# Optimization experiments

Hardware: AMD Instinct MI355X
Metric: run time of the kernel (lower is better)

## Reference

```python
import jax, jax.numpy as jnp
import numpy as np

N = 40000      # num_ent
INIT = 100     # init_dim
D = 200        # gcn_dim
F = 4          # num_factors
E = 800000     # num edges (incl. inverses)
NREL = 800     # num_rel * 2
L = 2          # gcn_layer
B = 2048       # batch of (sub, rel)
H2 = D // 2    # CLUBSample hidden_size // 2
NPAIR = F * (F - 1) // 2  # 6 MI discriminators


def setup_inputs() -> dict:
    key = jax.random.key(0)
    ks = jax.random.split(key, 24)
    inp = {}
    inp['sub'] = jax.random.randint(ks[0], (B,), 0, N)
    inp['rel'] = jax.random.randint(ks[1], (B,), 0, NREL)
    inp['edge_index'] = jax.random.randint(ks[2], (2, E), 0, N)
    inp['edge_type'] = jax.random.randint(ks[3], (E,), 0, NREL)
    inp['perm'] = jax.random.permutation(ks[4], B)
    s = 0.05
    inp['init_embed'] = jax.random.normal(ks[5], (N, INIT), jnp.float32) * s
    inp['init_rel'] = jax.random.normal(ks[6], (NREL, D), jnp.float32) * s
    stdv = 1.0 / np.sqrt(F * D)
    inp['pca_w'] = jax.random.uniform(ks[7], (INIT, F * D), jnp.float32, -stdv, stdv)
    inp['pca_b'] = jax.random.uniform(ks[8], (F * D,), jnp.float32, -stdv, stdv)
    inp['cw_w'] = jax.random.normal(ks[9], (D, D), jnp.float32) * 0.1
    inp['w_rel'] = jax.random.normal(ks[10], (L, D, D), jnp.float32) * s
    # CLUBSample MLPs stacked over the NPAIR discriminators
    inp['mu_w1'] = jax.random.normal(ks[11], (NPAIR, D, H2), jnp.float32) * s
    inp['mu_b1'] = jnp.zeros((NPAIR, H2), jnp.float32)
    inp['mu_w2'] = jax.random.normal(ks[12], (NPAIR, H2, D), jnp.float32) * s
    inp['mu_b2'] = jnp.zeros((NPAIR, D), jnp.float32)
    inp['lv_w1'] = jax.random.normal(ks[13], (NPAIR, D, H2), jnp.float32) * s
    inp['lv_b1'] = jnp.zeros((NPAIR, H2), jnp.float32)
    inp['lv_w2'] = jax.random.normal(ks[14], (NPAIR, H2, D), jnp.float32) * s
    inp['lv_b2'] = jnp.zeros((NPAIR, D), jnp.float32)
    return inp


def _leaky(v):
    return jnp.where(v > 0, v, 0.2 * v)


def _club(xi, yj, yj_perm, w1, b1, w2, b2, v1, c1, v2, c2):
    # CLUBSample.forward: MI upper bound between factor i and factor j
    mu = jax.nn.relu(xi @ w1 + b1) @ w2 + b2
    logvar = jnp.tanh(jax.nn.relu(xi @ v1 + c1) @ v2 + c2)
    inv_var = jnp.exp(-logvar)
    pos = -(mu - yj) ** 2 * inv_var
    neg = -(mu - yj_perm) ** 2 * inv_var
    return (pos.sum(-1) - neg.sum(-1)).mean() / 2.0


def _encode(init_embed, init_rel, pca_w, pca_b, cw_w, w_rel, edge_index, edge_type):
    # SparseInputLinear + tanh -> [N, F, D]
    x = jnp.tanh(init_embed @ pca_w + pca_b).reshape(N, F, D)
    # CalculateWeight: leaky_relu matmul then softmax over the factor axis
    kw = _leaky(x.reshape(-1, D) @ cw_w).reshape(N, F, D)
    kw = jax.nn.softmax(kw, axis=1)
    r = init_rel
    src, dst = edge_index[0], edge_index[1]
    for l in range(L):
        r_edge = r[edge_type]  # [E, D]
        aggs = []
        for k in range(F):  # small fixed loop over factors to bound memory
            m = x[src, k] * r_edge                              # [E, D] messages
            logit = _leaky(jnp.sum(m * x[dst, k], axis=-1))     # [E] attention logits
            mx = jax.ops.segment_max(logit, dst, num_segments=N)
            a = jnp.exp(logit - mx[dst])
            den = jax.ops.segment_sum(a, dst, num_segments=N)
            a = a / (den[dst] + 1e-16)                          # per-dst softmax
            aggs.append(jax.ops.segment_sum(a[:, None] * m, dst, num_segments=N))
        agg = jnp.stack(aggs, axis=1)                           # [N, F, D]
        x = jnp.tanh(agg) * kw                                  # factor routing
        r = r @ w_rel[l]
    return x, r


def reference(sub, rel, edge_index, edge_type, perm,
              init_embed, init_rel, pca_w, pca_b, cw_w, w_rel,
              mu_w1, mu_b1, mu_w2, mu_b2, lv_w1, lv_b1, lv_w2, lv_b2):
    x, _ = _encode(init_embed, init_rel, pca_w, pca_b, cw_w, w_rel, edge_index, edge_type)
    sub_emb = x[sub].reshape(B, F * D)
    rel_emb = jnp.tile(init_rel[rel], (1, F))  # index_select + repeat(1, F)
    mi_loss = jnp.float32(0.0)
    cnt = 0
    for i in range(F):
        for j in range(i + 1, F):
            xi = sub_emb[:, i * D:(i + 1) * D]
            yj = sub_emb[:, j * D:(j + 1) * D]
            mi_loss = mi_loss + _club(xi, yj, yj[perm],
                                      mu_w1[cnt], mu_b1[cnt], mu_w2[cnt], mu_b2[cnt],
                                      lv_w1[cnt], lv_b1[cnt], lv_w2[cnt], lv_b2[cnt])
            cnt += 1
    return (sub_emb, rel_emb, x, mi_loss)
```

## Files before the change

### kernel.cpp

```cpp
#include <hip/hip_runtime.h>
#include <hip/hip_bf16.h>

#define N_NODES 40000
#define INIT_D  100
#define DD      200
#define FF      4
#define EE      800000
#define NRELS   800
#define BB      2048
#define H2D     100
#define FD      800
#define RPAD    224
#define XPAD    256

typedef __hip_bfloat16 bf16;
typedef unsigned char u8;
typedef unsigned int u32;
typedef float floatx2 __attribute__((ext_vector_type(2)));
typedef float floatx4 __attribute__((ext_vector_type(4)));
typedef u32 u32x2 __attribute__((ext_vector_type(2)));

#define XSCALE 256.f
#define XINV   (1.f / 256.f)

__device__ __forceinline__ float b2f(bf16 v) { return __bfloat162float(v); }

__device__ __forceinline__ void fp8x4_dec(u32 q, float* o) {
    floatx2 lo = __builtin_amdgcn_cvt_pk_f32_fp8((int)q, false);
    floatx2 hi = __builtin_amdgcn_cvt_pk_f32_fp8((int)q, true);
    o[0] = lo.x; o[1] = lo.y; o[2] = hi.x; o[3] = hi.y;
}

__device__ __forceinline__ u32 fp8x4_enc(float v0, float v1, float v2, float v3) {
    int o = 0;
    o = __builtin_amdgcn_cvt_pk_fp8_f32(v0, v1, o, false);
    o = __builtin_amdgcn_cvt_pk_fp8_f32(v2, v3, o, true);
    return (u32)o;
}

__device__ __forceinline__ float red16(float v) {
    int t;
    t = __builtin_amdgcn_update_dpp(0, __float_as_int(v), 0xB1, 0xF, 0xF, true);
    v += __int_as_float(t);
    t = __builtin_amdgcn_update_dpp(0, __float_as_int(v), 0x4E, 0xF, 0xF, true);
    v += __int_as_float(t);
    t = __builtin_amdgcn_update_dpp(0, __float_as_int(v), 0x124, 0xF, 0xF, true);
    v += __int_as_float(t);
    t = __builtin_amdgcn_update_dpp(0, __float_as_int(v), 0x128, 0xF, 0xF, true);
    v += __int_as_float(t);
    return v;
}

__global__ __launch_bounds__(256) void zero_kernel(int* count, double* loss, u8* pad0, u8* pad1) {
    int idx = blockIdx.x * 256 + threadIdx.x;
    if (idx < N_NODES) count[idx] = 0;
    if (idx == 0) *loss = 0.0;
    if (idx < 64 && pad0) ((u32*)pad0)[idx] = 0u;
    if (idx < 64 && pad1) ((u32*)pad1)[idx] = 0u;
}

__global__ __launch_bounds__(64) void pca_kernel(const float* __restrict__ emb,
                                                 const float* __restrict__ pw,
                                                 const float* __restrict__ pb,
                                                 u8* __restrict__ xq,
                                                 float* __restrict__ xf,
                                                 int mode) {
    __shared__ float es[INIT_D][18];
    int r0 = blockIdx.y * 16;
    int c  = blockIdx.x * 64 + threadIdx.x;
    for (int idx = threadIdx.x; idx < 16 * INIT_D; idx += 64) {
        int r = idx / INIT_D, k = idx % INIT_D;
        es[k][r] = emb[(size_t)(r0 + r) * INIT_D + k];
    }
    __syncthreads();
    if (c >= FD) return;
    floatx2 acc[8];
#pragma unroll
    for (int i = 0; i < 8; i++) acc[i] = (floatx2){0.f, 0.f};
    for (int k = 0; k < INIT_D; k++) {
        float w = pw[k * FD + c];
        floatx2 w2 = (floatx2){w, w};
#pragma unroll
        for (int i = 0; i < 8; i++) acc[i] += *(const floatx2*)&es[k][2 * i] * w2;
    }
    float bias = pb[c];
#pragma unroll
    for (int r = 0; r < 16; r++) {
        float a = (r & 1) ? acc[r >> 1].y : acc[r >> 1].x;
        float v = tanhf(a + bias);
        if (mode == 0) {
            int t8 = __builtin_amdgcn_cvt_pk_fp8_f32(v * XSCALE, 0.f, 0, false);
            xq[(size_t)(r0 + r) * FD + c] = (u8)(t8 & 0xFF);
        } else {
            xf[(size_t)(r0 + r) * FD + c] = v;
        }
    }
}

__global__ __launch_bounds__(256) void kw_fast(const u8* __restrict__ xr,
                                               const float* __restrict__ cw,
                                               u8* __restrict__ kwout) {
    __shared__ float as[4][16][100];
    int wv = threadIdx.x >> 6, lane = threadIdx.x & 63;
    int g = blockIdx.x * 4 + wv;
    size_t rowbase = (size_t)g * 16;
    floatx2 acc[16][2];
#pragma unroll
    for (int r = 0; r < 16; r++) {
        acc[r][0] = (floatx2){0.f, 0.f};
        acc[r][1] = (floatx2){0.f, 0.f};
    }
    int cc[4], cl[4];
#pragma unroll
    for (int i = 0; i < 4; i++) { cc[i] = i * 64 + lane; cl[i] = cc[i] < DD ? cc[i] : DD - 1; }
    for (int kc = 0; kc < 2; kc++) {
        for (int j = lane; j < 400; j += 64) {
            int rr = j / 25, k4 = (j % 25) * 4;
            u32 q = *(const u32*)(xr + (rowbase + rr) * DD + kc * 100 + k4);
            float dv[4];
            fp8x4_dec(q, dv);
            *(floatx4*)&as[wv][rr][k4] = (floatx4){dv[0], dv[1], dv[2], dv[3]};
        }
        for (int kk = 0; kk < 100; kk += 4) {
            floatx2 w01[4], w23[4];
#pragma unroll
            for (int j = 0; j < 4; j++) {
                const float* cwp = cw + (size_t)(kc * 100 + kk + j) * DD;
                w01[j] = (floatx2){cwp[cl[0]], cwp[cl[1]]};
                w23[j] = (floatx2){cwp[cl[2]], cwp[cl[3]]};
            }
#pragma unroll
            for (int r = 0; r < 16; r++) {
                floatx4 av = *(const floatx4*)&as[wv][r][kk];
                acc[r][0] += av.x * w01[0]; acc[r][1] += av.x * w23[0];
                acc[r][0] += av.y * w01[1]; acc[r][1] += av.y * w23[1];
                acc[r][0] += av.z * w01[2]; acc[r][1] += av.z * w23[2];
                acc[r][0] += av.w * w01[3]; acc[r][1] += av.w * w23[3];
            }
        }
    }
#define GA(r, i) ((i) == 0 ? acc[r][0].x : (i) == 1 ? acc[r][0].y : (i) == 2 ? acc[r][1].x : acc[r][1].y)
#pragma unroll
    for (int j = 0; j < 4; j++) {
        int n = g * 4 + j;
#pragma unroll
        for (int i = 0; i < 4; i++) {
            if (cc[i] >= DD) continue;
            float v0 = GA(j * 4 + 0, i) * XINV, v1 = GA(j * 4 + 1, i) * XINV;
            float v2 = GA(j * 4 + 2, i) * XINV, v3 = GA(j * 4 + 3, i) * XINV;
            v0 = v0 > 0.f ? v0 : 0.2f * v0;
            v1 = v1 > 0.f ? v1 : 0.2f * v1;
            v2 = v2 > 0.f ? v2 : 0.2f * v2;
            v3 = v3 > 0.f ? v3 : 0.2f * v3;
            float m = fmaxf(fmaxf(v0, v1), fmaxf(v2, v3));
            float e0 = __expf(v0 - m), e1 = __expf(v1 - m);
            float e2 = __expf(v2 - m), e3 = __expf(v3 - m);
            float inv = 1.f / (e0 + e1 + e2 + e3);
            size_t base = (size_t)n * FD + cc[i];
            kwout[base]          = (u8)(e0 * inv * 255.f + 0.5f);
            kwout[base + DD]     = (u8)(e1 * inv * 255.f + 0.5f);
            kwout[base + 2 * DD] = (u8)(e2 * inv * 255.f + 0.5f);
            kwout[base + 3 * DD] = (u8)(e3 * inv * 255.f + 0.5f);
        }
    }
#undef GA
}

__global__ __launch_bounds__(256) void kw_old(const float* __restrict__ x,
                                              const float* __restrict__ cw,
                                              u8* __restrict__ kw) {
    int wave = threadIdx.x >> 6, lane = threadIdx.x & 63;
    int n = blockIdx.x * 4 + wave;
    const float* xp = x + (size_t)n * FD;
    float acc[4][4];
#pragma unroll
    for (int f = 0; f < 4; f++)
#pragma unroll
        for (int i = 0; i < 4; i++) acc[f][i] = 0.f;
    for (int k = 0; k < DD; k++) {
        float xv0 = xp[k], xv1 = xp[DD + k];
        float xv2 = xp[2 * DD + k], xv3 = xp[3 * DD + k];
#pragma unroll
        for (int i = 0; i < 4; i++) {
            int d = i * 64 + lane;
            float w = (d < DD) ? cw[k * DD + d] : 0.f;
            acc[0][i] += xv0 * w; acc[1][i] += xv1 * w;
            acc[2][i] += xv2 * w; acc[3][i] += xv3 * w;
        }
    }
    u8* kwp = kw + (size_t)n * FD;
#pragma unroll
    for (int i = 0; i < 4; i++) {
        int d = i * 64 + lane;
        if (d >= DD) continue;
        float v0 = acc[0][i], v1 = acc[1][i], v2 = acc[2][i], v3 = acc[3][i];
        v0 = v0 > 0.f ? v0 : 0.2f * v0;
        v1 = v1 > 0.f ? v1 : 0.2f * v1;
        v2 = v2 > 0.f ? v2 : 0.2f * v2;
        v3 = v3 > 0.f ? v3 : 0.2f * v3;
        float m = fmaxf(fmaxf(v0, v1), fmaxf(v2, v3));
        float e0 = __expf(v0 - m), e1 = __expf(v1 - m), e2 = __expf(v2 - m), e3 = __expf(v3 - m);
        float inv = 1.f / (e0 + e1 + e2 + e3);
        kwp[d]          = (u8)(e0 * inv * 255.f + 0.5f);
        kwp[DD + d]     = (u8)(e1 * inv * 255.f + 0.5f);
        kwp[2 * DD + d] = (u8)(e2 * inv * 255.f + 0.5f);
        kwp[3 * DD + d] = (u8)(e3 * inv * 255.f + 0.5f);
    }
}

__global__ __launch_bounds__(256) void count_kernel(const int* __restrict__ dst, int* count) {
    int e = blockIdx.x * 256 + threadIdx.x;
    atomicAdd(&count[dst[e]], 1);
}

__global__ __launch_bounds__(1024) void scan_kernel(int* __restrict__ count, int* __restrict__ offs) {
    __shared__ int wsums[16];
    __shared__ int carry_s;
    int tid = threadIdx.x;
    int wv = tid >> 6, lane = tid & 63;
    if (tid == 0) { carry_s = 0; offs[0] = 0; }
    __syncthreads();
    for (int base = 0; base < 40960; base += 1024) {
        int i = base + tid;
        int v = (i < N_NODES) ? count[i] : 0;
        if (i < N_NODES) count[i] = 0;
        int x = v;
#pragma unroll
        for (int off = 1; off < 64; off <<= 1) {
            int y = __shfl_up(x, off, 64);
            if (lane >= off) x += y;
        }
        if (lane == 63) wsums[wv] = x;
        __syncthreads();
        if (wv == 0) {
            int s = (lane < 16) ? wsums[lane] : 0;
#pragma unroll
            for (int off = 1; off < 16; off <<= 1) {
                int y = __shfl_up(s, off, 64);
                if (lane >= off) s += y;
            }
            if (lane < 16) wsums[lane] = s;
        }
        __syncthreads();
        int add = carry_s + (wv > 0 ? wsums[wv - 1] : 0);
        int incl = x + add;
        if (i < N_NODES) offs[i + 1] = incl;
        __syncthreads();
        if (tid == 1023) carry_s = incl;
        __syncthreads();
    }
}

__global__ __launch_bounds__(256) void scatter_kernel(const int* __restrict__ src,
                                                      const int* __restrict__ dst,
                                                      const int* __restrict__ etyp,
                                                      const int* __restrict__ offs,
                                                      int* cursor,
                                                      u32* __restrict__ ep) {
    int e = blockIdx.x * 256 + threadIdx.x;
    int d = dst[e];
    int p = offs[d] + atomicAdd(&cursor[d], 1);
    ep[p] = ((u32)etyp[e] << 16) | (u32)src[e];
}

__global__ __launch_bounds__(256) void r0pad_kernel(const float* __restrict__ r0,
                                                    float* __restrict__ rp) {
    int idx = blockIdx.x * 256 + threadIdx.x;
    int n = idx / RPAD, d = idx % RPAD;
    rp[idx] = (d < DD) ? r0[n * DD + d] : 0.f;
}

__global__ __launch_bounds__(256) void rmul_kernel(const float* __restrict__ r0,
                                                   const float* __restrict__ w,
                                                   float* __restrict__ r1) {
    __shared__ float row[DD];
    int n = blockIdx.x;
    if (threadIdx.x < DD) row[threadIdx.x] = r0[n * DD + threadIdx.x];
    __syncthreads();
    int d = threadIdx.x;
    if (d < DD) {
        float acc = 0.f;
        for (int k = 0; k < DD; k++) acc += row[k] * w[k * DD + d];
        r1[n * RPAD + d] = acc;
    } else if (d < RPAD) {
        r1[n * RPAD + d] = 0.f;
    }
}

__global__ __launch_bounds__(256) void agg_fp8(const u8* __restrict__ xin,
                                               const u8* __restrict__ kwv,
                                               const float* __restrict__ r,
                                               const int* __restrict__ offs,
                                               const u32* __restrict__ ep,
                                               u8* __restrict__ xoq,
                                               float* __restrict__ xof,
                                               int mode) {
    int n    = blockIdx.x * 4 + (threadIdx.x >> 6);
    int lane = threadIdx.x & 63;
    int f    = lane >> 4;
    int k    = lane & 15;
    bool act = k < 13;
    int xoff = f * DD + k * 16;
    int roffc = k * 16; if (roffc > 200) roffc = 200;

    float xdf[16];
    {
        const u8* xdp = xin + (size_t)n * FD + xoff;
        u32x2 a = *(const u32x2*)xdp;
        u32x2 b = *(const u32x2*)(xdp + 8);
        fp8x4_dec(a.x, xdf); fp8x4_dec(a.y, xdf + 4);
        fp8x4_dec(b.x, xdf + 8); fp8x4_dec(b.y, xdf + 12);
    }
    floatx2 xd2[8];
#pragma unroll
    for (int j = 0; j < 8; j++) xd2[j] = (floatx2){xdf[2 * j], xdf[2 * j + 1]};

    floatx2 A[8];
#pragma unroll
    for (int j = 0; j < 8; j++) A[j] = (floatx2){0.f, 0.f};
    float Sm = 0.f;

    int e0 = offs[n], e1 = offs[n + 1];

#define ISSUE(QA, QB, R0, R1, R2, R3, JJ) do {                                  \
    u32 wrd_ = (u32)__builtin_amdgcn_readlane((int)epv, (JJ));                  \
    int s_ = (int)(wrd_ & 0xFFFFu), t_ = (int)(wrd_ >> 16);                     \
    const u8* xsp_ = xin + (size_t)s_ * FD;                                     \
    const float* rp_ = r + (size_t)t_ * RPAD + roffc;                           \
    QA = *(const u32x2*)(xsp_ + xoff);                                          \
    QB = *(const u32x2*)(xsp_ + xoff + 8);                                      \
    const floatx4* r4_ = (const floatx4*)rp_;                                   \
    R0 = r4_[0]; R1 = r4_[1]; R2 = r4_[2]; R3 = r4_[3];                         \
} while (0)

#define COMPUTE(QA, QB, R0, R1, R2, R3) do {                                    \
    float xsf_[16];                                                             \
    fp8x4_dec(QA.x, xsf_);     fp8x4_dec(QA.y, xsf_ + 4);                       \
    fp8x4_dec(QB.x, xsf_ + 8); fp8x4_dec(QB.y, xsf_ + 12);                      \
    floatx2 rr_[8];                                                             \
    rr_[0] = (floatx2){R0.x, R0.y}; rr_[1] = (floatx2){R0.z, R0.w};             \
    rr_[2] = (floatx2){R1.x, R1.y}; rr_[3] = (floatx2){R1.z, R1.w};             \
    rr_[4] = (floatx2){R2.x, R2.y}; rr_[5] = (floatx2){R2.z, R2.w};             \
    rr_[6] = (floatx2){R3.x, R3.y}; rr_[7] = (floatx2){R3.z, R3.w};             \
    floatx2 mm_[8];                                                             \
    floatx2 ps_ = (floatx2){0.f, 0.f};                                          \
    _Pragma("unroll")                                                           \
    for (int j_ = 0; j_ < 8; j_++) {                                            \
        floatx2 xs2_ = (floatx2){xsf_[2 * j_], xsf_[2 * j_ + 1]};               \
        mm_[j_] = xs2_ * rr_[j_];                                               \
        ps_ += mm_[j_] * xd2[j_];                                               \
    }                                                                           \
    float p_ = red16(ps_.x + ps_.y);                                            \
    float q_ = p_ * (XINV * XINV);                                              \
    float lg_ = fmaxf(q_, 0.2f * q_);                                           \
    float wg_ = __expf(lg_);                                                    \
    Sm += wg_;                                                                  \
    floatx2 w2_ = (floatx2){wg_, wg_};                                          \
    _Pragma("unroll")                                                           \
    for (int j_ = 0; j_ < 8; j_++) A[j_] += w2_ * mm_[j_];                      \
} while (0)

    for (int cb = e0; cb < e1; cb += 64) {
        int cnt = e1 - cb; if (cnt > 64) cnt = 64;
        u32 epv = ep[cb + (lane < cnt ? lane : cnt - 1)];
        u32x2 qaA, qbA, qaB, qbB;
        floatx4 rA0, rA1, rA2, rA3, rB0, rB1, rB2, rB3;
        ISSUE(qaA, qbA, rA0, rA1, rA2, rA3, 0);
        if (cnt > 1) ISSUE(qaB, qbB, rB0, rB1, rB2, rB3, 1);
        int m2 = cnt & ~1;
        for (int ii = 0; ii < m2; ii += 2) {
            COMPUTE(qaA, qbA, rA0, rA1, rA2, rA3);
            if (ii + 2 < cnt) ISSUE(qaA, qbA, rA0, rA1, rA2, rA3, ii + 2);
            COMPUTE(qaB, qbB, rB0, rB1, rB2, rB3);
            if (ii + 3 < cnt) ISSUE(qaB, qbB, rB0, rB1, rB2, rB3, ii + 3);
        }
        if (cnt & 1) COMPUTE(qaA, qbA, rA0, rA1, rA2, rA3);
    }
#undef ISSUE
#undef COMPUTE

    float inv = 1.f / (Sm + 1e-16f);
    u32 kws[4];
    {
        const u8* kwp = kwv + (size_t)n * FD + xoff;
        u32x2 ka = *(const u32x2*)kwp;
        u32x2 kb = *(const u32x2*)(kwp + 8);
        kws[0] = ka.x; kws[1] = ka.y; kws[2] = kb.x; kws[3] = kb.y;
    }
    float v[16];
#pragma unroll
    for (int j = 0; j < 16; j++) {
        float kv = (float)((kws[j >> 2] >> ((j & 3) * 8)) & 0xFF) * (1.f / 255.f);
        float Aj = (j & 1) ? A[j >> 1].y : A[j >> 1].x;
        v[j] = tanhf(Aj * inv * XINV) * kv;
    }
    if (mode == 0) {
        if (act) {
            u32 o0 = fp8x4_enc(v[0] * XSCALE, v[1] * XSCALE, v[2] * XSCALE, v[3] * XSCALE);
            u32 o1 = fp8x4_enc(v[4] * XSCALE, v[5] * XSCALE, v[6] * XSCALE, v[7] * XSCALE);
            u32 o2 = fp8x4_enc(v[8] * XSCALE, v[9] * XSCALE, v[10] * XSCALE, v[11] * XSCALE);
            u32 o3 = fp8x4_enc(v[12] * XSCALE, v[13] * XSCALE, v[14] * XSCALE, v[15] * XSCALE);
            u8* op = xoq + (size_t)n * FD + xoff;
            *(u32x2*)op = (u32x2){o0, o1};
            if (k < 12) *(u32x2*)(op + 8) = (u32x2){o2, o3};
        }
    } else {
        if (act) {
            float* op = xof + (size_t)n * FD + xoff;
            *(floatx4*)op       = (floatx4){v[0], v[1], v[2], v[3]};
            *(floatx4*)(op + 4) = (floatx4){v[4], v[5], v[6], v[7]};
            if (k < 12) {
                *(floatx4*)(op + 8)  = (floatx4){v[8], v[9], v[10], v[11]};
                *(floatx4*)(op + 12) = (floatx4){v[12], v[13], v[14], v[15]};
            }
        }
    }
}

__global__ __launch_bounds__(256) void agg_sliced(const float* __restrict__ xall,
                                                  const u8* __restrict__ kw,
                                                  const float* __restrict__ r,
                                                  const int* __restrict__ offs,
                                                  const u32* __restrict__ ep,
                                                  bf16* __restrict__ xtmp,
                                                  int f) {
    int n    = blockIdx.x * 4 + (threadIdx.x >> 6);
    int lane = threadIdx.x & 63;
    const float* xdp = xall + (size_t)n * FD + f * DD;
    float xd[4];
#pragma unroll
    for (int i = 0; i < 4; i++) {
        int d = i * 64 + lane;
        xd[i] = (d < DD) ? xdp[d] : 0.f;
    }
    float M = -INFINITY, S = 0.f;
    float A0 = 0.f, A1 = 0.f, A2 = 0.f, A3 = 0.f;
    int e0 = offs[n], e1 = offs[n + 1];
    for (int e = e0; e < e1; ++e) {
        u32 wrd = ep[e];
        int s = wrd & 0xFFFF, t = wrd >> 16;
        const float* xsp = xall + (size_t)s * FD + f * DD;
        const float* rp = r + (size_t)t * RPAD;
        float mm[4];
        float p = 0.f;
#pragma unroll
        for (int i = 0; i < 4; i++) {
            int d = i * 64 + lane;
            float xs = (d < DD) ? xsp[d] : 0.f;
            float rrv = (d < DD) ? rp[d] : 0.f;
            mm[i] = xs * rrv;
            p += mm[i] * xd[i];
        }
#pragma unroll
        for (int o = 32; o > 0; o >>= 1) p += __shfl_xor(p, o, 64);
        float logit = p > 0.f ? p : 0.2f * p;
        float nm = fmaxf(M, logit);
        float sc = __expf(M - nm);
        float w  = __expf(logit - nm);
        S  = S * sc + w;
        A0 = A0 * sc + w * mm[0];
        A1 = A1 * sc + w * mm[1];
        A2 = A2 * sc + w * mm[2];
        A3 = A3 * sc + w * mm[3];
        M = nm;
    }
    float inv = 1.f / (S + 1e-16f);
    const u8* kwp = kw + (size_t)n * FD + f * DD;
    bf16* xo = xtmp + (size_t)n * DD;
    float A[4] = {A0, A1, A2, A3};
#pragma unroll
    for (int i = 0; i < 4; i++) {
        int d = i * 64 + lane;
        if (d < DD) {
            float kv = (float)kwp[d] * (1.f / 255.f);
            xo[d] = __float2bfloat16(tanhf(A[i] * inv) * kv);
        }
    }
}

__global__ __launch_bounds__(256) void copyback_kernel(const bf16* __restrict__ xtmp,
                                                       float* __restrict__ xall, int f) {
    int idx = blockIdx.x * 256 + threadIdx.x;
    int n = idx / DD, d = idx % DD;
    xall[(size_t)n * FD + f * DD + d] = b2f(xtmp[idx]);
}

__global__ __launch_bounds__(256) void subemb_kernel(const float* __restrict__ x,
                                                     const int* __restrict__ sub,
                                                     float* __restrict__ out) {
    int idx = blockIdx.x * 256 + threadIdx.x;
    int b = idx / FD, c = idx % FD;
    out[idx] = x[(size_t)sub[b] * FD + c];
}

__global__ __launch_bounds__(256) void relemb_kernel(const float* __restrict__ ir,
                                                     const int* __restrict__ rel,
                                                     float* __restrict__ out) {
    int idx = blockIdx.x * 256 + threadIdx.x;
    int b = idx / FD, d = idx % DD;
    out[idx] = ir[(size_t)rel[b] * DD + d];
}

__global__ __launch_bounds__(256) void club_kernel(const float* __restrict__ se,
                                                   const int* __restrict__ perm,
                                                   const float* __restrict__ mu_w1, const float* __restrict__ mu_b1,
                                                   const float* __restrict__ mu_w2, const float* __restrict__ mu_b2,
                                                   const float* __restrict__ lv_w1, const float* __restrict__ lv_b1,
                                                   const float* __restrict__ lv_w2, const float* __restrict__ lv_b2,
                                                   double* loss) {
    const int PI[6] = {0, 0, 0, 1, 1, 2};
    const int PJ[6] = {1, 2, 3, 2, 3, 3};
    int p = blockIdx.y;
    int i = PI[p], j = PJ[p];
    __shared__ float xi[DD], yj[DD], yjp[DD], h1m[H2D], h1v[H2D];
    __shared__ float wsum[4];
    float psum = 0.f;
    for (int rr = 0; rr < 8; ++rr) {
        int b = blockIdx.x * 8 + rr;
        int bp = perm[b];
        if (threadIdx.x < DD) {
            int t = threadIdx.x;
            xi[t]  = se[(size_t)b * FD + i * DD + t];
            yj[t]  = se[(size_t)b * FD + j * DD + t];
            yjp[t] = se[(size_t)bp * FD + j * DD + t];
        }
        __syncthreads();
        if (threadIdx.x < H2D) {
            int c = threadIdx.x;
            float a1 = mu_b1[p * H2D + c];
            float a2 = lv_b1[p * H2D + c];
            for (int d = 0; d < DD; d++) {
                float xv = xi[d];
                a1 += xv * mu_w1[(size_t)p * DD * H2D + d * H2D + c];
                a2 += xv * lv_w1[(size_t)p * DD * H2D + d * H2D + c];
            }
            h1m[c] = fmaxf(a1, 0.f);
            h1v[c] = fmaxf(a2, 0.f);
        }
        __syncthreads();
        if (threadIdx.x < DD) {
            int d = threadIdx.x;
            float m = mu_b2[p * DD + d];
            float v = lv_b2[p * DD + d];
            for (int c = 0; c < H2D; c++) {
                m += h1m[c] * mu_w2[(size_t)p * H2D * DD + c * DD + d];
                v += h1v[c] * lv_w2[(size_t)p * H2D * DD + c * DD + d];
            }
            float lv = tanhf(v);
            float ivr = __expf(-lv);
            float d1 = m - yj[d], d2 = m - yjp[d];
            psum += (d2 * d2 - d1 * d1) * ivr;
        }
        __syncthreads();
    }
    float v = psum;
#pragma unroll
    for (int o = 32; o > 0; o >>= 1) v += __shfl_xor(v, o, 64);
    if ((threadIdx.x & 63) == 0) wsum[threadIdx.x >> 6] = v;
    __syncthreads();
    if (threadIdx.x == 0) {
        double t = (double)wsum[0] + (double)wsum[1] + (double)wsum[2] + (double)wsum[3];
        atomicAdd(loss, t / (2.0 * (double)BB));
    }
}

__global__ void loss_out_kernel(const double* loss, float* out) {
    if (threadIdx.x == 0 && blockIdx.x == 0)
        out[0] = (float)(*loss);
}

extern "C" void kernel_launch(void* const* d_in, const int* in_sizes, int n_in,
                              void* d_out, int out_size, void* d_ws, size_t ws_size,
                              hipStream_t stream) {
    const int* sub  = (const int*)d_in[0];
    const int* rel  = (const int*)d_in[1];
    const int* eidx = (const int*)d_in[2];
    const int* etyp = (const int*)d_in[3];
    const int* perm = (const int*)d_in[4];
    const float* init_embed = (const float*)d_in[5];
    const float* init_rel   = (const float*)d_in[6];
    const float* pca_w = (const float*)d_in[7];
    const float* pca_b = (const float*)d_in[8];
    const float* cw_w  = (const float*)d_in[9];
    const float* w_rel = (const float*)d_in[10];
    const float* mu_w1 = (const float*)d_in[11];
    const float* mu_b1 = (const float*)d_in[12];
    const float* mu_w2 = (const float*)d_in[13];
    const float* mu_b2 = (const float*)d_in[14];
    const float* lv_w1 = (const float*)d_in[15];
    const float* lv_b1 = (const float*)d_in[16];
    const float* lv_w2 = (const float*)d_in[17];
    const float* lv_b2 = (const float*)d_in[18];

    float* out = (float*)d_out;
    const size_t OFF_SUB = 0;
    const size_t OFF_REL = 1638400;
    const size_t OFF_X   = 3276800;
    const size_t OFF_MI  = 35276800;
    float* xall = out + OFF_X;

    const int* src = eidx;
    const int* dst = eidx + EE;

    bool fast = (ws_size >= (size_t)101 * 1000 * 1000);

    char* w = (char*)d_ws;
    u8* xq0 = nullptr; u8* xq1 = nullptr; bf16* xtmp = nullptr;
    if (fast) {
        xq0 = (u8*)w; w += (size_t)N_NODES * FD + XPAD;
        xq1 = (u8*)w; w += (size_t)N_NODES * FD + XPAD;
    } else {
        xtmp = (bf16*)w; w += (size_t)N_NODES * DD * 2;
    }
    u8*   kwb  = (u8*)w;    w += (size_t)N_NODES * FD + XPAD;
    float* r0p = (float*)w; w += NRELS * RPAD * 4;
    float* r1  = (float*)w; w += NRELS * RPAD * 4;
    u32* ep    = (u32*)w;   w += EE * 4;
    int* count = (int*)w;   w += N_NODES * 4;
    int* offs  = (int*)w;   w += (N_NODES + 16) * 4;
    double* loss = (double*)w; w += 256;

    hipLaunchKernelGGL(zero_kernel, dim3(157), dim3(256), 0, stream, count, loss,
                       fast ? xq0 + (size_t)N_NODES * FD : nullptr,
                       fast ? xq1 + (size_t)N_NODES * FD : nullptr);
    hipLaunchKernelGGL(pca_kernel, dim3(13, 2500), dim3(64), 0, stream,
                       init_embed, pca_w, pca_b, xq0, xall, fast ? 0 : 1);
    if (fast) hipLaunchKernelGGL(kw_fast, dim3(2500), dim3(256), 0, stream, xq0, cw_w, kwb);
    else      hipLaunchKernelGGL(kw_old, dim3(10000), dim3(256), 0, stream, xall, cw_w, kwb);
    hipLaunchKernelGGL(count_kernel, dim3(3125), dim3(256), 0, stream, dst, count);
    hipLaunchKernelGGL(scan_kernel, dim3(1), dim3(1024), 0, stream, count, offs);
    hipLaunchKernelGGL(scatter_kernel, dim3(3125), dim3(256), 0, stream, src, dst, etyp, offs, count, ep);
    hipLaunchKernelGGL(r0pad_kernel, dim3(700), dim3(256), 0, stream, init_rel, r0p);
    hipLaunchKernelGGL(rmul_kernel, dim3(800), dim3(256), 0, stream, init_rel, w_rel, r1);

    if (fast) {
        hipLaunchKernelGGL(agg_fp8, dim3(10000), dim3(256), 0, stream,
                           xq0, kwb, r0p, offs, ep, xq1, (float*)nullptr, 0);
        hipLaunchKernelGGL(agg_fp8, dim3(10000), dim3(256), 0, stream,
                           xq1, kwb, r1, offs, ep, (u8*)nullptr, xall, 1);
    } else {
        for (int f = 0; f < FF; f++) {
            hipLaunchKernelGGL(agg_sliced, dim3(10000), dim3(256), 0, stream,
                               xall, kwb, r0p, offs, ep, xtmp, f);
            hipLaunchKernelGGL(copyback_kernel, dim3(31250), dim3(256), 0, stream, xtmp, xall, f);
        }
        for (int f = 0; f < FF; f++) {
            hipLaunchKernelGGL(agg_sliced, dim3(10000), dim3(256), 0, stream,
                               xall, kwb, r1, offs, ep, xtmp, f);
            hipLaunchKernelGGL(copyback_kernel, dim3(31250), dim3(256), 0, stream, xtmp, xall, f);
        }
    }

    hipLaunchKernelGGL(subemb_kernel, dim3(6400), dim3(256), 0, stream, xall, sub, out + OFF_SUB);
    hipLaunchKernelGGL(relemb_kernel, dim3(6400), dim3(256), 0, stream, init_rel, rel, out + OFF_REL);
    hipLaunchKernelGGL(club_kernel, dim3(256, 6), dim3(256), 0, stream, out + OFF_SUB, perm,
                       mu_w1, mu_b1, mu_w2, mu_b2, lv_w1, lv_b1, lv_w2, lv_b2, loss);
    hipLaunchKernelGGL(loss_out_kernel, dim3(1), dim3(64), 0, stream, loss, out + OFF_MI);
}
```

Measured before the change: 1.253 ms.

## Compute factor-routing weights with bf16 MFMA using hi/lo split of cw

Replaces the scalar FP32 kw_fast GEMM (x_factor @ cw_w followed by a 4-way softmax) with a kernel built on 16x16x32 bf16 MFMA instructions. A new pack kernel splits cw_w into high and low bf16 parts and lays them out in MFMA B-fragment order, so the weight precision stays close to fp32. The fp8 activations are decoded straight to bf16 in registers. The pack buffer reuses the edge-permutation workspace before the scatter kernel writes it, which adds a dependency on launch ordering.

```diff
diff --git a/kernel.cpp b/kernel.cpp
--- a/kernel.cpp
+++ b/kernel.cpp
@@ -15,10 +15,12 @@
 
 typedef __hip_bfloat16 bf16;
 typedef unsigned char u8;
+typedef unsigned short u16;
 typedef unsigned int u32;
 typedef float floatx2 __attribute__((ext_vector_type(2)));
 typedef float floatx4 __attribute__((ext_vector_type(4)));
 typedef u32 u32x2 __attribute__((ext_vector_type(2)));
+typedef short bshort8 __attribute__((ext_vector_type(8)));
 
 #define XSCALE 256.f
 #define XINV   (1.f / 256.f)
@@ -49,6 +51,15 @@
     t = __builtin_amdgcn_update_dpp(0, __float_as_int(v), 0x128, 0xF, 0xF, true);
     v += __int_as_float(t);
     return v;
+}
+
+__device__ __forceinline__ bshort8 fp8x8_bf16(u32x2 q) {
+    float f[8];
+    fp8x4_dec(q.x, f); fp8x4_dec(q.y, f + 4);
+    bshort8 r;
+#pragma unroll
+    for (int j = 0; j < 8; j++) r[j] = (short)(__float_as_uint(f[j]) >> 16);
+    return r;
 }
 
 __global__ __launch_bounds__(256) void zero_kernel(int* count, double* loss, u8* pad0, u8* pad1) {
@@ -97,73 +108,93 @@
     }
 }
 
-__global__ __launch_bounds__(256) void kw_fast(const u8* __restrict__ xr,
-                                               const float* __restrict__ cw,
+__global__ __launch_bounds__(256) void bpack_kernel(const float* __restrict__ cw,
+                                                    u16* __restrict__ bpH,
+                                                    u16* __restrict__ bpL) {
+    int w = (blockIdx.x * 256 + threadIdx.x) >> 6;
+    int lane = threadIdx.x & 63;
+    if (w >= 91) return;
+    int t = w / 7, s = w % 7;
+    int col = t * 16 + (lane & 15);
+    int g = lane >> 4;
+    bshort8 hv, lv;
+#pragma unroll
+    for (int j = 0; j < 8; j++) {
+        int k = s * 32 + g * 8 + j;
+        float v = (k < DD && col < DD) ? cw[k * DD + col] : 0.f;
+        u32 b = __float_as_uint(v);
+        u32 rb = b + 0x7FFFu + ((b >> 16) & 1u);
+        u16 h = (u16)(rb >> 16);
+        float hf = __uint_as_float(((u32)h) << 16);
+        float lo = v - hf;
+        u32 lb = __float_as_uint(lo);
+        lb += 0x7FFFu + ((lb >> 16) & 1u);
+        hv[j] = (short)h;
+        lv[j] = (short)(lb >> 16);
+    }
+    size_t base = ((size_t)w * 64 + lane) * 8;
+    *(bshort8*)(bpH + base) = hv;
+    *(bshort8*)(bpL + base) = lv;
+}
+
+__global__ __launch_bounds__(256) void kw_mfma(const u8* __restrict__ xq,
+                                               const u16* __restrict__ bpH,
+                                               const u16* __restrict__ bpL,
                                                u8* __restrict__ kwout) {
-    __shared__ float as[4][16][100];
     int wv = threadIdx.x >> 6, lane = threadIdx.x & 63;
-    int g = blockIdx.x * 4 + wv;
-    size_t rowbase = (size_t)g * 16;
-    floatx2 acc[16][2];
-#pragma unroll
-    for (int r = 0; r < 16; r++) {
-        acc[r][0] = (floatx2){0.f, 0.f};
-        acc[r][1] = (floatx2){0.f, 0.f};
-    }
-    int cc[4], cl[4];
-#pragma unroll
-    for (int i = 0; i < 4; i++) { cc[i] = i * 64 + lane; cl[i] = cc[i] < DD ? cc[i] : DD - 1; }
-    for (int kc = 0; kc < 2; kc++) {
-        for (int j = lane; j < 400; j += 64) {
-            int rr = j / 25, k4 = (j % 25) * 4;
-            u32 q = *(const u32*)(xr + (rowbase + rr) * DD + kc * 100 + k4);
-            float dv[4];
-            fp8x4_dec(q, dv);
-            *(floatx4*)&as[wv][rr][k4] = (floatx4){dv[0], dv[1], dv[2], dv[3]};
-        }
-        for (int kk = 0; kk < 100; kk += 4) {
-            floatx2 w01[4], w23[4];
-#pragma unroll
-            for (int j = 0; j < 4; j++) {
-                const float* cwp = cw + (size_t)(kc * 100 + kk + j) * DD;
-                w01[j] = (floatx2){cwp[cl[0]], cwp[cl[1]]};
-                w23[j] = (floatx2){cwp[cl[2]], cwp[cl[3]]};
-            }
-#pragma unroll
-            for (int r = 0; r < 16; r++) {
-                floatx4 av = *(const floatx4*)&as[wv][r][kk];
-                acc[r][0] += av.x * w01[0]; acc[r][1] += av.x * w23[0];
-                acc[r][0] += av.y * w01[1]; acc[r][1] += av.y * w23[1];
-                acc[r][0] += av.z * w01[2]; acc[r][1] += av.z * w23[2];
-                acc[r][0] += av.w * w01[3]; acc[r][1] += av.w * w23[3];
-            }
-        }
-    }
-#define GA(r, i) ((i) == 0 ? acc[r][0].x : (i) == 1 ? acc[r][0].y : (i) == 2 ? acc[r][1].x : acc[r][1].y)
-#pragma unroll
-    for (int j = 0; j < 4; j++) {
-        int n = g * 4 + j;
-#pragma unroll
-        for (int i = 0; i < 4; i++) {
-            if (cc[i] >= DD) continue;
-            float v0 = GA(j * 4 + 0, i) * XINV, v1 = GA(j * 4 + 1, i) * XINV;
-            float v2 = GA(j * 4 + 2, i) * XINV, v3 = GA(j * 4 + 3, i) * XINV;
+    int Mbase = blockIdx.x * 128 + wv * 32;
+    int g = lane >> 4, c16 = lane & 15;
+    floatx4 acc[2][13];
+#pragma unroll
+    for (int m = 0; m < 2; m++)
+#pragma unroll
+        for (int t = 0; t < 13; t++) acc[m][t] = (floatx4){0.f, 0.f, 0.f, 0.f};
+
+    const u8* a0p = xq + (size_t)(Mbase + c16) * DD + g * 8;
+    const u8* a1p = a0p + 16 * DD;
+
+    for (int s = 0; s < 7; s++) {
+        u32x2 qa = *(const u32x2*)(a0p + s * 32);
+        u32x2 qb = *(const u32x2*)(a1p + s * 32);
+        bshort8 a0 = fp8x8_bf16(qa);
+        bshort8 a1 = fp8x8_bf16(qb);
+        const u16* hp = bpH + s * 512 + lane * 8;
+        const u16* lp = bpL + s * 512 + lane * 8;
+#pragma unroll
+        for (int t = 0; t < 13; t++) {
+            bshort8 bh = *(const bshort8*)(hp + (size_t)t * 3584);
+            bshort8 bl = *(const bshort8*)(lp + (size_t)t * 3584);
+            acc[0][t] = __builtin_amdgcn_mfma_f32_16x16x32_bf16(a0, bh, acc[0][t], 0, 0, 0);
+            acc[1][t] = __builtin_amdgcn_mfma_f32_16x16x32_bf16(a1, bh, acc[1][t], 0, 0, 0);
+            acc[0][t] = __builtin_amdgcn_mfma_f32_16x16x32_bf16(a0, bl, acc[0][t], 0, 0, 0);
+            acc[1][t] = __builtin_amdgcn_mfma_f32_16x16x32_bf16(a1, bl, acc[1][t], 0, 0, 0);
+        }
+    }
+
+    int rq = g * 4;
+#pragma unroll
+    for (int m = 0; m < 2; m++) {
+#pragma unroll
+        for (int t = 0; t < 13; t++) {
+            int col = t * 16 + c16;
+            if (col >= DD) continue;
+            floatx4 a = acc[m][t];
+            float v0 = a.x * XINV, v1 = a.y * XINV, v2 = a.z * XINV, v3 = a.w * XINV;
             v0 = v0 > 0.f ? v0 : 0.2f * v0;
             v1 = v1 > 0.f ? v1 : 0.2f * v1;
             v2 = v2 > 0.f ? v2 : 0.2f * v2;
             v3 = v3 > 0.f ? v3 : 0.2f * v3;
-            float m = fmaxf(fmaxf(v0, v1), fmaxf(v2, v3));
-            float e0 = __expf(v0 - m), e1 = __expf(v1 - m);
-            float e2 = __expf(v2 - m), e3 = __expf(v3 - m);
+            float mx = fmaxf(fmaxf(v0, v1), fmaxf(v2, v3));
+            float e0 = __expf(v0 - mx), e1 = __expf(v1 - mx);
+            float e2 = __expf(v2 - mx), e3 = __expf(v3 - mx);
             float inv = 1.f / (e0 + e1 + e2 + e3);
-            size_t base = (size_t)n * FD + cc[i];
-            kwout[base]          = (u8)(e0 * inv * 255.f + 0.5f);
-            kwout[base + DD]     = (u8)(e1 * inv * 255.f + 0.5f);
-            kwout[base + 2 * DD] = (u8)(e2 * inv * 255.f + 0.5f);
-            kwout[base + 3 * DD] = (u8)(e3 * inv * 255.f + 0.5f);
-        }
-    }
-#undef GA
+            size_t base = (size_t)(Mbase + m * 16 + rq) * DD + col;
+            kwout[base]           = (u8)(e0 * inv * 255.f + 0.5f);
+            kwout[base + DD]      = (u8)(e1 * inv * 255.f + 0.5f);
+            kwout[base + 2 * DD]  = (u8)(e2 * inv * 255.f + 0.5f);
+            kwout[base + 3 * DD]  = (u8)(e3 * inv * 255.f + 0.5f);
+        }
+    }
 }
 
 __global__ __launch_bounds__(256) void kw_old(const float* __restrict__ x,
@@ -620,12 +651,16 @@
     int* offs  = (int*)w;   w += (N_NODES + 16) * 4;
     double* loss = (double*)w; w += 256;
 
+    u16* bpH = (u16*)ep;
+    u16* bpL = bpH + 13 * 7 * 64 * 8;
+
     hipLaunchKernelGGL(zero_kernel, dim3(157), dim3(256), 0, stream, count, loss,
                        fast ? xq0 + (size_t)N_NODES * FD : nullptr,
                        fast ? xq1 + (size_t)N_NODES * FD : nullptr);
+    if (fast) hipLaunchKernelGGL(bpack_kernel, dim3(23), dim3(256), 0, stream, cw_w, bpH, bpL);
     hipLaunchKernelGGL(pca_kernel, dim3(13, 2500), dim3(64), 0, stream,
                        init_embed, pca_w, pca_b, xq0, xall, fast ? 0 : 1);
-    if (fast) hipLaunchKernelGGL(kw_fast, dim3(2500), dim3(256), 0, stream, xq0, cw_w, kwb);
+    if (fast) hipLaunchKernelGGL(kw_mfma, dim3(1250), dim3(256), 0, stream, xq0, bpH, bpL, kwb);
     else      hipLaunchKernelGGL(kw_old, dim3(10000), dim3(256), 0, stream, xall, cw_w, kwb);
     hipLaunchKernelGGL(count_kernel, dim3(3125), dim3(256), 0, stream, dst, count);
     hipLaunchKernelGGL(scan_kernel, dim3(1), dim3(1024), 0, stream, count, offs);
```

Result: faster. 1.215 ms (-3.1%).
